# Performance work log

Measured on AMD Instinct MI355X. Metric: run time of the kernel, lower is better.

Reference implementation:

```python
import jax, jax.numpy as jnp
import numpy as np

OFFSETS = (1, 2, 4, 8, 16, 64, 96, 192, 384, 512, 768, 1024)
J = 12
J_LARGE = 8  # offsets with index >= 4 use phase rotation


def _shift(x, d):
    """Return x shifted so out[..., n, :] = x[..., n-d, :]; zeros where n < d.
    Shift is along axis 2 (the sequence axis of [B,H,N,...])."""
    pad = [(0, 0)] * x.ndim
    pad[2] = (d, 0)
    return jnp.pad(x, pad)[:, :, : x.shape[2]]


def setup_inputs() -> dict:
    key = jax.random.key(0)
    ks = jax.random.split(key, 9)
    B, H, N, HD = 2, 16, 4096, 64
    f = jnp.float32
    q = jax.random.normal(ks[0], (B, H, N, HD), f)
    k = jax.random.normal(ks[1], (B, H, N, HD), f)
    v = jax.random.normal(ks[2], (B, H, N, HD), f)
    pb = jax.random.normal(ks[3], (J, H), f) * 0.1          # per-offset per-head score bias
    se = jax.random.normal(ks[4], (J, HD), f) * 0.1         # per-offset score embedding
    phase_base = jax.random.normal(ks[5], (J_LARGE, H, 2), f) * 0.1
    phase_gain = jax.random.normal(ks[6], (J_LARGE, H, 2), f) * 0.1
    y_pre = jax.random.normal(ks[7], (B, H, N, 2), f)       # query-side phase features
    z_pre = jax.random.normal(ks[8], (B, H, N, 2), f)       # key-side phase features
    return dict(q=q, k=k, v=v, pb=pb, se=se, phase_base=phase_base,
                phase_gain=phase_gain, y_pre=y_pre, z_pre=z_pre)


def reference(q, k, v, pb, se, phase_base, phase_gain, y_pre, z_pre):
    B, H, N, HD = q.shape
    sc = 1.0 / float(np.sqrt(HD))
    n_idx = jnp.arange(N)

    # --- scores over the J fixed causal offsets: s_i[n] = (q_n . (k_{n-d} + se_i)) * sc + pb[i,h]
    scores = []
    for i, d in enumerate(OFFSETS):
        ks_ = _shift(k, d)  # key at n - d
        s = (jnp.einsum('bhnd,bhnd->bhn', q, ks_)
             + jnp.einsum('bhnd,d->bhn', q, se[i])) * sc
        s = s + pb[i][None, :, None]
        valid = (n_idx >= d)[None, None, :]
        scores.append(jnp.where(valid, s, -jnp.inf))
    scores = jnp.stack(scores, axis=-1)  # [B,H,N,J]

    lse = jax.nn.logsumexp(scores, axis=-1)            # [B,H,N]
    safe_lse = jnp.where(jnp.isfinite(lse), lse, 0.0)  # rows with no valid offset -> alpha = 0
    alpha = jnp.exp(scores - safe_lse[..., None])      # [B,H,N,J]; -inf scores give exactly 0

    # --- weighted sum of (phase-rotated) values
    out = jnp.zeros_like(q)
    for i, d in enumerate(OFFSETS):
        vs = _shift(v, d)  # value at n - d: [B,H,N,HD]
        if i >= 4:
            pi = i - 4
            zs = _shift(z_pre, d)  # key-side phase features at n - d: [B,H,N,2]
            # theta_p = base[pi,h,p] + gain[pi,h,p] * y_pre[n,p] * z_pre[n-d,p]
            theta = (phase_base[pi][None, :, None, :]
                     + phase_gain[pi][None, :, None, :] * y_pre * zs)  # [B,H,N,2]
            c, s_ = jnp.cos(theta), jnp.sin(theta)
            v0, v1, v2, v3 = vs[..., 0], vs[..., 1], vs[..., 2], vs[..., 3]
            rot = jnp.stack([c[..., 0] * v0 - s_[..., 0] * v1,
                             s_[..., 0] * v0 + c[..., 0] * v1,
                             c[..., 1] * v2 - s_[..., 1] * v3,
                             s_[..., 1] * v2 + c[..., 1] * v3], axis=-1)
            vs = jnp.concatenate([rot, vs[..., 4:]], axis=-1)
        out = out + alpha[..., i:i + 1] * vs
    return out
```

## Files before the change

kernel.cpp:

```cpp
#include <hip/hip_runtime.h>


namespace {

constexpr int J   = 12;
constexpr int B_  = 2;
constexpr int H_  = 16;
constexpr int N_  = 4096;
constexpr int HD_ = 64;
constexpr int OFFS[J] = {1, 2, 4, 8, 16, 64, 96, 192, 384, 512, 768, 1024};

__global__ __launch_bounds__(256) void dsqg_kernel(
    const float* __restrict__ q, const float* __restrict__ k,
    const float* __restrict__ v, const float* __restrict__ pb,
    const float* __restrict__ se, const float* __restrict__ phase_base,
    const float* __restrict__ phase_gain, const float* __restrict__ y_pre,
    const float* __restrict__ z_pre, float* __restrict__ out)
{
    const int raw = blockIdx.x;
    const int per = gridDim.x >> 3;
    const int wid = (raw & 7) * per + (raw >> 3);

    const int bh    = wid >> 8;
    const int chunk = wid & 255;
    const int h     = bh & (H_ - 1);

    const int lane = threadIdx.x & 63;
    const int wave = threadIdx.x >> 6;
    const int grp  = lane & 15;
    const int n    = chunk * 16 + wave * 4 + (lane >> 4);

    const size_t base4 = (size_t)bh * N_ * (HD_ / 4);
    const float4* q4 = (const float4*)q + base4;
    const float4* k4 = (const float4*)k + base4;
    const float4* v4 = (const float4*)v + base4;
    float4*       o4 = (float4*)out + base4;

    const float4 qr = q4[(size_t)n * 16 + grp];

    int m[J];
    bool ok[J];
#pragma unroll
    for (int i = 0; i < J; ++i) {
        ok[i] = (n >= OFFS[i]);
        m[i]  = ok[i] ? (n - OFFS[i]) : 0;
    }

    float2 zr[8];
    float2 yp = make_float2(0.f, 0.f);
    if (grp == 0) {
        yp = ((const float2*)y_pre)[(size_t)bh * N_ + n];
#pragma unroll
        for (int pi = 0; pi < 8; ++pi)
            zr[pi] = ((const float2*)z_pre)[(size_t)bh * N_ + m[pi + 4]];
    }

    float4 kr[J];
#pragma unroll
    for (int i = 0; i < J; ++i) kr[i] = k4[(size_t)m[i] * 16 + grp];

    float p[J];
#pragma unroll
    for (int i = 0; i < J; ++i) {
        const float4 seg = ((const float4*)se)[i * 16 + grp];
        float t = qr.x * seg.x + qr.y * seg.y + qr.z * seg.z + qr.w * seg.w;
        t = fmaf(qr.x, kr[i].x, t);
        t = fmaf(qr.y, kr[i].y, t);
        t = fmaf(qr.z, kr[i].z, t);
        p[i] = fmaf(qr.w, kr[i].w, t);
    }

    float4 vr[J];
#pragma unroll
    for (int i = 0; i < J; ++i) vr[i] = v4[(size_t)m[i] * 16 + grp];

#pragma unroll
    for (int stage = 1; stage <= 8; stage <<= 1) {
#pragma unroll
        for (int i = 0; i < J; ++i) p[i] += __shfl_xor(p[i], stage);
    }

    const float sc = 0.125f;
    float e[J];
    float sum = 0.f;
#pragma unroll
    for (int i = 0; i < J; ++i) {
        const float si = fmaf(p[i], sc, pb[i * H_ + h]);
        e[i] = ok[i] ? __expf(si) : 0.f;
        sum += e[i];
    }

    if (grp == 0) {
#pragma unroll
        for (int pi = 0; pi < 8; ++pi) {
            const int i = pi + 4;
            const float b0 = phase_base[(pi * H_ + h) * 2 + 0];
            const float b1 = phase_base[(pi * H_ + h) * 2 + 1];
            const float g0 = phase_gain[(pi * H_ + h) * 2 + 0];
            const float g1 = phase_gain[(pi * H_ + h) * 2 + 1];
            const float th0 = fmaf(g0, yp.x * zr[pi].x, b0);
            const float th1 = fmaf(g1, yp.y * zr[pi].y, b1);
            const float c0 = __cosf(th0), s0 = __sinf(th0);
            const float c1 = __cosf(th1), s1 = __sinf(th1);
            const float v0 = vr[i].x, v1 = vr[i].y, v2 = vr[i].z, v3 = vr[i].w;
            vr[i].x = c0 * v0 - s0 * v1;
            vr[i].y = s0 * v0 + c0 * v1;
            vr[i].z = c1 * v2 - s1 * v3;
            vr[i].w = s1 * v2 + c1 * v3;
        }
    }

    float4 acc = make_float4(0.f, 0.f, 0.f, 0.f);
#pragma unroll
    for (int i = 0; i < J; ++i) {
        acc.x = fmaf(e[i], vr[i].x, acc.x);
        acc.y = fmaf(e[i], vr[i].y, acc.y);
        acc.z = fmaf(e[i], vr[i].z, acc.z);
        acc.w = fmaf(e[i], vr[i].w, acc.w);
    }

    float4 res;
    if (n >= 1) {
        const float inv = 1.0f / sum;
        res = make_float4(acc.x * inv, acc.y * inv, acc.z * inv, acc.w * inv);
    } else {
        res = make_float4(0.f, 0.f, 0.f, 0.f);
    }
    o4[(size_t)n * 16 + grp] = res;
}

}

extern "C" void kernel_launch(void* const* d_in, const int* in_sizes, int n_in,
                              void* d_out, int out_size, void* d_ws, size_t ws_size,
                              hipStream_t stream) {
    const float* q          = (const float*)d_in[0];
    const float* k          = (const float*)d_in[1];
    const float* v          = (const float*)d_in[2];
    const float* pb         = (const float*)d_in[3];
    const float* se         = (const float*)d_in[4];
    const float* phase_base = (const float*)d_in[5];
    const float* phase_gain = (const float*)d_in[6];
    const float* y_pre      = (const float*)d_in[7];
    const float* z_pre      = (const float*)d_in[8];
    float* out              = (float*)d_out;

    const int positions = B_ * H_ * N_;
    const int blocks    = positions / 16;
    dsqg_kernel<<<blocks, 256, 0, stream>>>(q, k, v, pb, se, phase_base,
                                            phase_gain, y_pre, z_pre, out);
}
```

Baseline: 194.7 us.

## Use DPP row reductions, 32-bit byte offsets, and hoist all K/V loads early

Replaces the 48 __shfl_xor cross-lane reductions (LDS bpermute traffic) with DPP quad_perm and row_ror adds inside each 16-lane row. Addressing moves to 32-bit byte offsets so all K and V gathers can be issued up front, before the score math. Other changes: se is folded into k before the dot product, division becomes a hardware reciprocal, and launch bounds now request 3 blocks per CU. Holding all 24 float4 loads live at once raises register pressure, and the reciprocal gives slightly different rounding.

```diff
diff --git a/kernel.cpp b/kernel.cpp
--- a/kernel.cpp
+++ b/kernel.cpp
@@ -10,7 +10,14 @@
 constexpr int HD_ = 64;
 constexpr int OFFS[J] = {1, 2, 4, 8, 16, 64, 96, 192, 384, 512, 768, 1024};
 
-__global__ __launch_bounds__(256) void dsqg_kernel(
+template <int CTRL>
+__device__ __forceinline__ float dpp_add(float x) {
+    int s = __builtin_amdgcn_update_dpp(0, __builtin_bit_cast(int, x),
+                                        CTRL, 0xF, 0xF, false);
+    return x + __builtin_bit_cast(float, s);
+}
+
+__global__ __launch_bounds__(256, 3) void dsqg_kernel(
     const float* __restrict__ q, const float* __restrict__ k,
     const float* __restrict__ v, const float* __restrict__ pb,
     const float* __restrict__ se, const float* __restrict__ phase_base,
@@ -30,54 +37,64 @@
     const int grp  = lane & 15;
     const int n    = chunk * 16 + wave * 4 + (lane >> 4);
 
-    const size_t base4 = (size_t)bh * N_ * (HD_ / 4);
-    const float4* q4 = (const float4*)q + base4;
-    const float4* k4 = (const float4*)k + base4;
-    const float4* v4 = (const float4*)v + base4;
-    float4*       o4 = (float4*)out + base4;
+    const size_t bhbytes = (size_t)bh * (N_ * HD_ * 4);
+    const char* qb = (const char*)q + bhbytes;
+    const char* kb = (const char*)k + bhbytes;
+    const char* vb = (const char*)v + bhbytes;
+    char*       ob = (char*)out + bhbytes;
 
-    const float4 qr = q4[(size_t)n * 16 + grp];
+    const uint32_t gb   = (uint32_t)grp << 4;
+    const uint32_t rowb = ((uint32_t)n << 8) + gb;
 
-    int m[J];
+    const float4 qr = *(const float4*)(qb + rowb);
+
     bool ok[J];
+    uint32_t offb[J];
 #pragma unroll
     for (int i = 0; i < J; ++i) {
-        ok[i] = (n >= OFFS[i]);
-        m[i]  = ok[i] ? (n - OFFS[i]) : 0;
+        ok[i]   = (n >= OFFS[i]);
+        offb[i] = ok[i] ? (rowb - ((uint32_t)OFFS[i] << 8)) : gb;
     }
+
+    float4 kr[J];
+#pragma unroll
+    for (int i = 0; i < J; ++i) kr[i] = *(const float4*)(kb + offb[i]);
+
+    float4 vr[J];
+#pragma unroll
+    for (int i = 0; i < J; ++i) vr[i] = *(const float4*)(vb + offb[i]);
 
     float2 zr[8];
     float2 yp = make_float2(0.f, 0.f);
     if (grp == 0) {
-        yp = ((const float2*)y_pre)[(size_t)bh * N_ + n];
+        const char* yb = (const char*)y_pre + (size_t)bh * (N_ * 8);
+        const char* zb = (const char*)z_pre + (size_t)bh * (N_ * 8);
+        const uint32_t nb8 = (uint32_t)n << 3;
+        yp = *(const float2*)(yb + nb8);
 #pragma unroll
-        for (int pi = 0; pi < 8; ++pi)
-            zr[pi] = ((const float2*)z_pre)[(size_t)bh * N_ + m[pi + 4]];
+        for (int pi = 0; pi < 8; ++pi) {
+            const uint32_t zo =
+                ok[pi + 4] ? (nb8 - ((uint32_t)OFFS[pi + 4] << 3)) : 0u;
+            zr[pi] = *(const float2*)(zb + zo);
+        }
     }
-
-    float4 kr[J];
-#pragma unroll
-    for (int i = 0; i < J; ++i) kr[i] = k4[(size_t)m[i] * 16 + grp];
 
     float p[J];
 #pragma unroll
     for (int i = 0; i < J; ++i) {
         const float4 seg = ((const float4*)se)[i * 16 + grp];
-        float t = qr.x * seg.x + qr.y * seg.y + qr.z * seg.z + qr.w * seg.w;
-        t = fmaf(qr.x, kr[i].x, t);
-        t = fmaf(qr.y, kr[i].y, t);
-        t = fmaf(qr.z, kr[i].z, t);
-        p[i] = fmaf(qr.w, kr[i].w, t);
+        float t = qr.x * (kr[i].x + seg.x);
+        t = fmaf(qr.y, kr[i].y + seg.y, t);
+        t = fmaf(qr.z, kr[i].z + seg.z, t);
+        p[i] = fmaf(qr.w, kr[i].w + seg.w, t);
     }
 
-    float4 vr[J];
 #pragma unroll
-    for (int i = 0; i < J; ++i) vr[i] = v4[(size_t)m[i] * 16 + grp];
-
-#pragma unroll
-    for (int stage = 1; stage <= 8; stage <<= 1) {
-#pragma unroll
-        for (int i = 0; i < J; ++i) p[i] += __shfl_xor(p[i], stage);
+    for (int i = 0; i < J; ++i) {
+        p[i] = dpp_add<0xB1>(p[i]);
+        p[i] = dpp_add<0x4E>(p[i]);
+        p[i] = dpp_add<0x124>(p[i]);
+        p[i] = dpp_add<0x128>(p[i]);
     }
 
     const float sc = 0.125f;
@@ -121,12 +138,12 @@
 
     float4 res;
     if (n >= 1) {
-        const float inv = 1.0f / sum;
+        const float inv = __builtin_amdgcn_rcpf(sum);
         res = make_float4(acc.x * inv, acc.y * inv, acc.z * inv, acc.w * inv);
     } else {
         res = make_float4(0.f, 0.f, 0.f, 0.f);
     }
-    o4[(size_t)n * 16 + grp] = res;
+    *(float4*)(ob + rowb) = res;
 }
 
 }
```

New measurement: 190.7 us. -2.0%, faster.
